# Optimization experiments

Hardware: AMD Instinct MI355X
Metric: run time of the kernel (lower is better)

The kernel has to match this reference:

```python
import jax, jax.numpy as jnp
import numpy as np

B, DIM, H, W = 4, 512, 64, 64
HEADS = 8
MAX_FREQ = 10000.0


def _rope_cos_sin(h, w, head_dim, dtype):
    # 2D RoPE: first quarter of half_dim uses row position, second quarter uses col position
    half = head_dim // 2
    quarter = half // 2
    pos_h = jnp.arange(h, dtype=dtype)
    pos_w = jnp.arange(w, dtype=dtype)
    gh, gw = jnp.meshgrid(pos_h, pos_w, indexing='ij')
    pos = jnp.stack([gh.ravel(), gw.ravel()], axis=-1)  # [N, 2]
    freqs = 1.0 / (MAX_FREQ ** (jnp.arange(quarter, dtype=dtype) / quarter))  # [quarter]
    ang_x = pos[:, 0:1] * freqs  # [N, quarter]
    ang_y = pos[:, 1:2] * freqs  # [N, quarter]
    cos = jnp.concatenate([jnp.cos(ang_x), jnp.cos(ang_y)], axis=-1)  # [N, half]
    sin = jnp.concatenate([jnp.sin(ang_x), jnp.sin(ang_y)], axis=-1)  # [N, half]
    return cos, sin


def _apply_rope(x, cos, sin):
    # x: [B, heads, N, head_dim]; cos/sin: [N, head_dim//2]
    d = x.shape[-1] // 2
    x1, x2 = x[..., :d], x[..., d:]
    return jnp.concatenate([x1 * cos - x2 * sin, x1 * sin + x2 * cos], axis=-1)


def setup_inputs() -> dict:
    key = jax.random.key(0)
    kx, kq, kp = jax.random.split(key, 3)
    x = jax.random.normal(kx, (B, DIM, H, W), dtype=jnp.float32)
    w_qkv = jax.random.normal(kq, (3 * DIM, DIM), dtype=jnp.float32) * (DIM ** -0.5)
    w_proj = jax.random.normal(kp, (DIM, DIM), dtype=jnp.float32) * (DIM ** -0.5)
    return {"x": x, "w_qkv": w_qkv, "w_proj": w_proj}


def reference(x, w_qkv, w_proj):
    Bb, C, Hh, Ww = x.shape
    heads = HEADS
    hd = C // heads
    N = Hh * Ww
    # 1x1 conv (bias-free) == channel-wise linear
    qkv = jnp.einsum('bchw,oc->bohw', x, w_qkv)  # [B, 3C, H, W]
    qkv = qkv.reshape(Bb, 3, heads, hd, Hh, Ww).transpose(1, 0, 2, 4, 5, 3)  # [3, B, heads, H, W, hd]
    q = qkv[0].reshape(Bb, heads, N, hd)
    k = qkv[1].reshape(Bb, heads, N, hd)
    v = qkv[2].reshape(Bb, heads, N, hd)
    cos, sin = _rope_cos_sin(Hh, Ww, hd, x.dtype)
    q = _apply_rope(q, cos, sin)
    k = _apply_rope(k, cos, sin)
    scale = hd ** -0.5
    attn = jax.nn.softmax(jnp.einsum('bhnd,bhmd->bhnm', q, k) * scale, axis=-1)  # [B, heads, N, N]
    out = jnp.einsum('bhnm,bhmd->bhnd', attn, v)  # [B, heads, N, hd]
    out = out.reshape(Bb, heads, Hh, Ww, hd).transpose(0, 1, 4, 2, 3).reshape(Bb, C, Hh, Ww)
    return jnp.einsum('bchw,oc->bohw', out, w_proj)
```

## Files before the change

### kernel.cpp

```cpp
#include <hip/hip_runtime.h>
#include <math.h>

#define B_    4
#define CDIM  512
#define HEADS 8
#define HD    64
#define NN    4096
#define QSZ   ((size_t)B_*HEADS*NN*HD)
#define SCALE_Q 0.18033688011112042f

typedef __attribute__((ext_vector_type(8))) short short8;
typedef __attribute__((ext_vector_type(4))) float f32x4;
typedef __attribute__((ext_vector_type(16))) float f32x16;
union U4S8 { uint4 u; short8 s; };

__device__ inline unsigned pk(float a, float b) {
    unsigned ua = __float_as_uint(a), ub = __float_as_uint(b);
    ua += 0x7FFFu + ((ua >> 16) & 1u);
    ub += 0x7FFFu + ((ub >> 16) & 1u);
    return (ua >> 16) | (ub & 0xFFFF0000u);
}
__device__ inline unsigned short bf16_1(float a) {
    unsigned ua = __float_as_uint(a);
    ua += 0x7FFFu + ((ua >> 16) & 1u);
    return (unsigned short)(ua >> 16);
}
__device__ inline unsigned cvtpk(float a, float b) {
    unsigned r;
    asm("v_cvt_pk_bf16_f32 %0, %1, %2" : "=v"(r) : "v"(a), "v"(b));
    return r;
}

__device__ inline void load_lds16(const unsigned short* g, unsigned short* l) {
    __builtin_amdgcn_global_load_lds(
        (const __attribute__((address_space(1))) unsigned int*)g,
        (__attribute__((address_space(3))) unsigned int*)l, 16, 0, 0);
}

__global__ void conv_w_kernel(const float* __restrict__ wq, const float* __restrict__ wp,
                              unsigned short* __restrict__ wqb, unsigned short* __restrict__ wpb) {
    int id = blockIdx.x * 256 + threadIdx.x;
    const float* src; unsigned short* dst; size_t off; float sc = 1.0f;
    if (id < 98304) { src = wq; dst = wqb; off = (size_t)id * 8; if (off < 262144) sc = SCALE_Q; }
    else            { src = wp; dst = wpb; off = (size_t)(id - 98304) * 8; }
    float4 a = *(const float4*)(src + off);
    float4 b = *(const float4*)(src + off + 4);
    uint4 u;
    u.x = pk(a.x * sc, a.y * sc); u.y = pk(a.z * sc, a.w * sc);
    u.z = pk(b.x * sc, b.y * sc); u.w = pk(b.z * sc, b.w * sc);
    *(uint4*)(dst + off) = u;
}

__global__ void rope_table_kernel(float* __restrict__ ct, float* __restrict__ st) {
    int id = blockIdx.x * 256 + threadIdx.x;
    int j = id >> 12, n = id & 4095;
    int i = j & 15;
    float pos = (j < 16) ? (float)(n >> 6) : (float)(n & 63);
    float freq = exp2f(-(float)i * 0.8304820237218406f);
    float ang = pos * freq;
    ct[id] = cosf(ang);
    st[id] = sinf(ang);
}

__global__ __launch_bounds__(256) void transpose_x_kernel(
        const float* __restrict__ x, unsigned short* __restrict__ xt) {
    __shared__ unsigned short T[64 * 72];
    int t = threadIdx.x;
    int b = blockIdx.z, c0 = blockIdx.y * 64, n0 = blockIdx.x * 64;
    const float* xb = x + ((size_t)b * CDIM + c0) * NN + n0;
    int crow = t >> 2, nseg = t & 3;
#pragma unroll
    for (int g = 0; g < 4; ++g) {
        float4 f = *(const float4*)(xb + (size_t)crow * NN + nseg * 16 + g * 4);
        int nb = nseg * 16 + g * 4;
        T[(nb + 0) * 72 + crow] = bf16_1(f.x);
        T[(nb + 1) * 72 + crow] = bf16_1(f.y);
        T[(nb + 2) * 72 + crow] = bf16_1(f.z);
        T[(nb + 3) * 72 + crow] = bf16_1(f.w);
    }
    __syncthreads();
    unsigned short* xo = xt + ((size_t)b * NN + n0) * CDIM + c0;
    int nrow = t >> 2, cseg = t & 3;
    uint4 u0 = *(uint4*)(T + nrow * 72 + cseg * 16);
    uint4 u1 = *(uint4*)(T + nrow * 72 + cseg * 16 + 8);
    *(uint4*)(xo + (size_t)nrow * CDIM + cseg * 16)     = u0;
    *(uint4*)(xo + (size_t)nrow * CDIM + cseg * 16 + 8) = u1;
}

__global__ __launch_bounds__(256, 2) void qkv_mfma_kernel(
        const unsigned short* __restrict__ xt, const unsigned short* __restrict__ wq,
        unsigned short* __restrict__ qbf, unsigned short* __restrict__ kbf,
        unsigned short* __restrict__ vt,
        const float* __restrict__ ct, const float* __restrict__ st) {
    __shared__ unsigned short smem[8192];
    int t = threadIdx.x;
    int lane = t & 63, w = t >> 6;
    int qlo = lane & 15, quad = lane >> 4;
    int b = blockIdx.z, o0 = blockIdx.y * 128, n0 = blockIdx.x * 128;
    const unsigned short* xb = xt + (size_t)b * NN * CDIM;
    int row = t >> 2, seg = t & 3;
    int wn = (w & 1) * 64, wo = (w >> 1) * 64;

    f32x4 acc[4][4];
#pragma unroll
    for (int i = 0; i < 4; ++i)
#pragma unroll
        for (int j = 0; j < 4; ++j) acc[i][j] = f32x4{0.f, 0.f, 0.f, 0.f};

    for (int k0 = 0; k0 < 512; k0 += 32) {
        __syncthreads();
        load_lds16(xb + (size_t)(n0 + row) * 512 + k0 + seg * 8,        smem + t * 8);
        load_lds16(xb + (size_t)(n0 + 64 + row) * 512 + k0 + seg * 8,   smem + 2048 + t * 8);
        load_lds16(wq + (size_t)(o0 + row) * 512 + k0 + seg * 8,        smem + 4096 + t * 8);
        load_lds16(wq + (size_t)(o0 + 64 + row) * 512 + k0 + seg * 8,   smem + 6144 + t * 8);
        __syncthreads();
        U4S8 af[4], bf[4];
#pragma unroll
        for (int mt = 0; mt < 4; ++mt)
            af[mt].u = *(const uint4*)(smem + (wn + 16 * mt + qlo) * 32 + quad * 8);
#pragma unroll
        for (int nt = 0; nt < 4; ++nt)
            bf[nt].u = *(const uint4*)(smem + 4096 + (wo + 16 * nt + qlo) * 32 + quad * 8);
#pragma unroll
        for (int mt = 0; mt < 4; ++mt)
#pragma unroll
            for (int nt = 0; nt < 4; ++nt)
                acc[mt][nt] = __builtin_amdgcn_mfma_f32_16x16x32_bf16(
                    af[mt].s, bf[nt].s, acc[mt][nt], 0, 0, 0);
    }

    int og = o0 + wo;
    int s = og >> 9;
    int h = (og & 511) >> 6;
    int bh = b * HEADS + h;
    if (s < 2) {
        unsigned short* dst = (s ? kbf : qbf) + (size_t)bh * NN * HD;
#pragma unroll
        for (int mt = 0; mt < 4; ++mt) {
            int nbase = n0 + wn + 16 * mt + 4 * quad;
#pragma unroll
            for (int ntp = 0; ntp < 2; ++ntp) {
                int j = 16 * ntp + qlo;
                float4 c4 = *(const float4*)(ct + (size_t)j * NN + nbase);
                float4 s4 = *(const float4*)(st + (size_t)j * NN + nbase);
                float cc[4] = {c4.x, c4.y, c4.z, c4.w};
                float ss[4] = {s4.x, s4.y, s4.z, s4.w};
#pragma unroll
                for (int r = 0; r < 4; ++r) {
                    float x1 = acc[mt][ntp][r], x2 = acc[mt][ntp + 2][r];
                    size_t base = (size_t)(nbase + r) * HD;
                    dst[base + j]      = bf16_1(x1 * cc[r] - x2 * ss[r]);
                    dst[base + j + 32] = bf16_1(x1 * ss[r] + x2 * cc[r]);
                }
            }
        }
    } else {
        unsigned short* dst = vt + (size_t)bh * HD * NN;
#pragma unroll
        for (int mt = 0; mt < 4; ++mt)
#pragma unroll
            for (int nt = 0; nt < 4; ++nt) {
                int d = 16 * nt + qlo;
                int n = n0 + wn + 16 * mt + 4 * quad;
                uint2 u;
                u.x = pk(acc[mt][nt][0], acc[mt][nt][1]);
                u.y = pk(acc[mt][nt][2], acc[mt][nt][3]);
                *(uint2*)(dst + (size_t)d * NN + n) = u;
            }
    }
}

#define EXP_GRP(Sv, MTQ, KSL, PA)                                        \
    {                                                                    \
        float p0 = __builtin_amdgcn_exp2f(Sv[8 * (KSL) + 0]);            \
        float p1 = __builtin_amdgcn_exp2f(Sv[8 * (KSL) + 1]);            \
        float p2 = __builtin_amdgcn_exp2f(Sv[8 * (KSL) + 2]);            \
        float p3 = __builtin_amdgcn_exp2f(Sv[8 * (KSL) + 3]);            \
        float p4 = __builtin_amdgcn_exp2f(Sv[8 * (KSL) + 4]);            \
        float p5 = __builtin_amdgcn_exp2f(Sv[8 * (KSL) + 5]);            \
        float p6 = __builtin_amdgcn_exp2f(Sv[8 * (KSL) + 6]);            \
        float p7 = __builtin_amdgcn_exp2f(Sv[8 * (KSL) + 7]);            \
        Lsum[MTQ] += ((p0 + p1) + (p2 + p3)) + ((p4 + p5) + (p6 + p7));  \
        PA.u.x = cvtpk(p0, p1); PA.u.y = cvtpk(p2, p3);                  \
        PA.u.z = cvtpk(p4, p5); PA.u.w = cvtpk(p6, p7);                  \
    }

__global__ __launch_bounds__(256, 2) void attn_kernel(
        const unsigned short* __restrict__ qbf, const unsigned short* __restrict__ kbf,
        const unsigned short* __restrict__ vt, unsigned short* __restrict__ aot) {
    __shared__ unsigned char smem[36864];
    int t = threadIdx.x;
    int lane = t & 63, w = t >> 6;
    int l31 = lane & 31, h = lane >> 5;
    int bb = blockIdx.z, hh = blockIdx.y;
    int bh = bb * HEADS + hh;
    int n0w = blockIdx.x * 256 + w * 64;

    U4S8 qf[2][4];
    const unsigned short* qg = qbf + ((size_t)bh * NN + n0w) * HD;
#pragma unroll
    for (int mtq = 0; mtq < 2; ++mtq)
#pragma unroll
        for (int ks = 0; ks < 4; ++ks)
            qf[mtq][ks].u = *(const uint4*)(qg + (size_t)(32 * mtq + l31) * 64 + 16 * ks + 8 * h);

    f32x16 Zv;
#pragma unroll
    for (int i = 0; i < 16; ++i) Zv[i] = 0.f;

    f32x16 O[2][2];
#pragma unroll
    for (int mtq = 0; mtq < 2; ++mtq)
#pragma unroll
        for (int ntd = 0; ntd < 2; ++ntd) O[mtq][ntd] = Zv;
    float Lsum[2] = {0.f, 0.f};

    const uint4* kg = (const uint4*)kbf + (size_t)bh * NN * 8;
    const uint4* vg = (const uint4*)vt  + (size_t)bh * 64 * 512;

    int rr0 = t >> 3, s8 = t & 7;
    int voff = 32 * (s8 >> 1) + 8 * (s8 & 1);

    const uint4* kp0 = kg + rr0 * 8 + s8;
    const uint4* kp1 = kg + (32 + rr0) * 8 + s8;
    const uint4* vp0 = vg + rr0 * 512 + s8;
    const uint4* vp1 = vg + (32 + rr0) * 512 + s8;

    unsigned char* kd0 = smem + rr0 * 144 + s8 * 16;
    unsigned char* kd1 = smem + (32 + rr0) * 144 + s8 * 16;
    unsigned char* vd0 = smem + 9216 + rr0 * 144 + voff;
    unsigned char* vd1 = smem + 9216 + (32 + rr0) * 144 + voff;

    uint4 kr0 = kp0[0], kr1 = kp1[0], vr0 = vp0[0], vr1 = vp1[0];
    kp0 += 512; kp1 += 512; vp0 += 8; vp1 += 8;
    *(uint4*)(kd0) = kr0;
    *(uint4*)(kd1) = kr1;
    *(uint2*)(vd0)      = make_uint2(vr0.x, vr0.y);
    *(uint2*)(vd0 + 16) = make_uint2(vr0.z, vr0.w);
    *(uint2*)(vd1)      = make_uint2(vr1.x, vr1.y);
    *(uint2*)(vd1 + 16) = make_uint2(vr1.z, vr1.w);
    kr0 = kp0[0]; kr1 = kp1[0]; vr0 = vp0[0]; vr1 = vp1[0];
    kp0 += 512; kp1 += 512; vp0 += 8; vp1 += 8;
    __syncthreads();

    for (int c = 0; c < NN / 64; ++c) {
        int bo = (c & 1) * 18432;
        const unsigned char* kb  = smem + bo;
        const unsigned char* vbb = smem + bo + 9216;
        int bo2 = bo ^ 18432;

        *(uint4*)(kd0 + bo2) = kr0;
        *(uint4*)(kd1 + bo2) = kr1;
        *(uint2*)(vd0 + bo2)      = make_uint2(vr0.x, vr0.y);
        *(uint2*)(vd0 + bo2 + 16) = make_uint2(vr0.z, vr0.w);
        *(uint2*)(vd1 + bo2)      = make_uint2(vr1.x, vr1.y);
        *(uint2*)(vd1 + bo2 + 16) = make_uint2(vr1.z, vr1.w);
        kr0 = kp0[0]; kr1 = kp1[0]; vr0 = vp0[0]; vr1 = vp1[0];
        kp0 += 512; kp1 += 512; vp0 += 8; vp1 += 8;

        __builtin_amdgcn_s_setprio(1);

        U4S8 ka0[4];
#pragma unroll
        for (int ks = 0; ks < 4; ++ks)
            ka0[ks].u = *(const uint4*)(kb + l31 * 144 + 32 * ks + 16 * h);
        f32x16 S0[2];
        S0[0] = __builtin_amdgcn_mfma_f32_32x32x16_bf16(ka0[0].s, qf[0][0].s, Zv, 0, 0, 0);
        S0[1] = __builtin_amdgcn_mfma_f32_32x32x16_bf16(ka0[0].s, qf[1][0].s, Zv, 0, 0, 0);
#pragma unroll
        for (int ks = 1; ks < 4; ++ks) {
            S0[0] = __builtin_amdgcn_mfma_f32_32x32x16_bf16(ka0[ks].s, qf[0][ks].s, S0[0], 0, 0, 0);
            S0[1] = __builtin_amdgcn_mfma_f32_32x32x16_bf16(ka0[ks].s, qf[1][ks].s, S0[1], 0, 0, 0);
        }

        U4S8 ka1[4];
#pragma unroll
        for (int ks = 0; ks < 4; ++ks)
            ka1[ks].u = *(const uint4*)(kb + (32 + l31) * 144 + 32 * ks + 16 * h);
        f32x16 S1[2];
        U4S8 paA[2][2];
        S1[0] = __builtin_amdgcn_mfma_f32_32x32x16_bf16(ka1[0].s, qf[0][0].s, Zv, 0, 0, 0);
        S1[1] = __builtin_amdgcn_mfma_f32_32x32x16_bf16(ka1[0].s, qf[1][0].s, Zv, 0, 0, 0);
        EXP_GRP(S0[0], 0, 0, paA[0][0]);
        S1[0] = __builtin_amdgcn_mfma_f32_32x32x16_bf16(ka1[1].s, qf[0][1].s, S1[0], 0, 0, 0);
        S1[1] = __builtin_amdgcn_mfma_f32_32x32x16_bf16(ka1[1].s, qf[1][1].s, S1[1], 0, 0, 0);
        EXP_GRP(S0[0], 0, 1, paA[1][0]);
        S1[0] = __builtin_amdgcn_mfma_f32_32x32x16_bf16(ka1[2].s, qf[0][2].s, S1[0], 0, 0, 0);
        S1[1] = __builtin_amdgcn_mfma_f32_32x32x16_bf16(ka1[2].s, qf[1][2].s, S1[1], 0, 0, 0);
        EXP_GRP(S0[1], 1, 0, paA[0][1]);
        S1[0] = __builtin_amdgcn_mfma_f32_32x32x16_bf16(ka1[3].s, qf[0][3].s, S1[0], 0, 0, 0);
        S1[1] = __builtin_amdgcn_mfma_f32_32x32x16_bf16(ka1[3].s, qf[1][3].s, S1[1], 0, 0, 0);
        EXP_GRP(S0[1], 1, 1, paA[1][1]);

        U4S8 paB[2][2];
        {
            U4S8 vb; vb.u = *(const uint4*)(vbb + l31 * 144 + 16 * h);
            O[0][0] = __builtin_amdgcn_mfma_f32_32x32x16_bf16(paA[0][0].s, vb.s, O[0][0], 0, 0, 0);
            O[1][0] = __builtin_amdgcn_mfma_f32_32x32x16_bf16(paA[0][1].s, vb.s, O[1][0], 0, 0, 0);
        }
        EXP_GRP(S1[0], 0, 0, paB[0][0]);
        {
            U4S8 vb; vb.u = *(const uint4*)(vbb + (32 + l31) * 144 + 16 * h);
            O[0][1] = __builtin_amdgcn_mfma_f32_32x32x16_bf16(paA[0][0].s, vb.s, O[0][1], 0, 0, 0);
            O[1][1] = __builtin_amdgcn_mfma_f32_32x32x16_bf16(paA[0][1].s, vb.s, O[1][1], 0, 0, 0);
        }
        EXP_GRP(S1[0], 0, 1, paB[1][0]);
        {
            U4S8 vb; vb.u = *(const uint4*)(vbb + l31 * 144 + 32 + 16 * h);
            O[0][0] = __builtin_amdgcn_mfma_f32_32x32x16_bf16(paA[1][0].s, vb.s, O[0][0], 0, 0, 0);
            O[1][0] = __builtin_amdgcn_mfma_f32_32x32x16_bf16(paA[1][1].s, vb.s, O[1][0], 0, 0, 0);
        }
        EXP_GRP(S1[1], 1, 0, paB[0][1]);
        {
            U4S8 vb; vb.u = *(const uint4*)(vbb + (32 + l31) * 144 + 32 + 16 * h);
            O[0][1] = __builtin_amdgcn_mfma_f32_32x32x16_bf16(paA[1][0].s, vb.s, O[0][1], 0, 0, 0);
            O[1][1] = __builtin_amdgcn_mfma_f32_32x32x16_bf16(paA[1][1].s, vb.s, O[1][1], 0, 0, 0);
        }
        EXP_GRP(S1[1], 1, 1, paB[1][1]);

        {
            U4S8 vb; vb.u = *(const uint4*)(vbb + l31 * 144 + 64 + 16 * h);
            O[0][0] = __builtin_amdgcn_mfma_f32_32x32x16_bf16(paB[0][0].s, vb.s, O[0][0], 0, 0, 0);
            O[1][0] = __builtin_amdgcn_mfma_f32_32x32x16_bf16(paB[0][1].s, vb.s, O[1][0], 0, 0, 0);
        }
        {
            U4S8 vb; vb.u = *(const uint4*)(vbb + (32 + l31) * 144 + 64 + 16 * h);
            O[0][1] = __builtin_amdgcn_mfma_f32_32x32x16_bf16(paB[0][0].s, vb.s, O[0][1], 0, 0, 0);
            O[1][1] = __builtin_amdgcn_mfma_f32_32x32x16_bf16(paB[0][1].s, vb.s, O[1][1], 0, 0, 0);
        }
        {
            U4S8 vb; vb.u = *(const uint4*)(vbb + l31 * 144 + 96 + 16 * h);
            O[0][0] = __builtin_amdgcn_mfma_f32_32x32x16_bf16(paB[1][0].s, vb.s, O[0][0], 0, 0, 0);
            O[1][0] = __builtin_amdgcn_mfma_f32_32x32x16_bf16(paB[1][1].s, vb.s, O[1][0], 0, 0, 0);
        }
        {
            U4S8 vb; vb.u = *(const uint4*)(vbb + (32 + l31) * 144 + 96 + 16 * h);
            O[0][1] = __builtin_amdgcn_mfma_f32_32x32x16_bf16(paB[1][0].s, vb.s, O[0][1], 0, 0, 0);
            O[1][1] = __builtin_amdgcn_mfma_f32_32x32x16_bf16(paB[1][1].s, vb.s, O[1][1], 0, 0, 0);
        }
        __builtin_amdgcn_s_setprio(0);
        __syncthreads();
    }

    float Linv[2];
#pragma unroll
    for (int mtq = 0; mtq < 2; ++mtq) {
        float l = Lsum[mtq] + __shfl_xor(Lsum[mtq], 32, 64);
        Linv[mtq] = 1.0f / l;
    }
    unsigned short* Tw = (unsigned short*)(smem + w * 4608);
    unsigned short* aob = aot + ((size_t)bb * NN) * CDIM + hh * 64;
#pragma unroll
    for (int mtq = 0; mtq < 2; ++mtq) {
        float iv[16];
#pragma unroll
        for (int r = 0; r < 16; ++r) {
            int src = (r & 3) + 8 * ((r >> 2) & 1) + 16 * (r >> 3) + 4 * h;
            iv[r] = __shfl(Linv[mtq], src, 64);
        }
#pragma unroll
        for (int rg = 0; rg < 2; ++rg) {
#pragma unroll
            for (int ntd = 0; ntd < 2; ++ntd)
#pragma unroll
                for (int rr = 0; rr < 8; ++rr) {
                    int r = 8 * rg + rr;
                    int q16 = (rr & 3) + 8 * (rr >> 2) + 4 * h;
                    Tw[q16 * 72 + 32 * ntd + l31] = bf16_1(O[mtq][ntd][r] * iv[r]);
                }
            int row = lane >> 2, cseg = lane & 3;
            uint4 u0 = *(uint4*)(Tw + row * 72 + cseg * 16);
            uint4 u1 = *(uint4*)(Tw + row * 72 + cseg * 16 + 8);
            unsigned short* arow = aob
                + (size_t)(n0w + 32 * mtq + 16 * rg + row) * CDIM + cseg * 16;
            *(uint4*)(arow)     = u0;
            *(uint4*)(arow + 8) = u1;
        }
    }
}

__global__ __launch_bounds__(256, 2) void proj_mfma_kernel(
        const unsigned short* __restrict__ aot, const unsigned short* __restrict__ wp,
        float* __restrict__ out) {
    __shared__ unsigned short smem[8192];
    int t = threadIdx.x;
    int lane = t & 63, w = t >> 6;
    int qlo = lane & 15, quad = lane >> 4;
    int b = blockIdx.z, o0 = blockIdx.y * 128, n0 = blockIdx.x * 128;
    const unsigned short* ab = aot + (size_t)b * NN * CDIM;
    int row = t >> 2, seg = t & 3;
    int wn = (w & 1) * 64, wo = (w >> 1) * 64;

    f32x4 acc[4][4];
#pragma unroll
    for (int i = 0; i < 4; ++i)
#pragma unroll
        for (int j = 0; j < 4; ++j) acc[i][j] = f32x4{0.f, 0.f, 0.f, 0.f};

    for (int k0 = 0; k0 < 512; k0 += 32) {
        __syncthreads();
        load_lds16(ab + (size_t)(n0 + row) * 512 + k0 + seg * 8,        smem + t * 8);
        load_lds16(ab + (size_t)(n0 + 64 + row) * 512 + k0 + seg * 8,   smem + 2048 + t * 8);
        load_lds16(wp + (size_t)(o0 + row) * 512 + k0 + seg * 8,        smem + 4096 + t * 8);
        load_lds16(wp + (size_t)(o0 + 64 + row) * 512 + k0 + seg * 8,   smem + 6144 + t * 8);
        __syncthreads();
        U4S8 af[4], bf[4];
#pragma unroll
        for (int mt = 0; mt < 4; ++mt)
            af[mt].u = *(const uint4*)(smem + (wn + 16 * mt + qlo) * 32 + quad * 8);
#pragma unroll
        for (int nt = 0; nt < 4; ++nt)
            bf[nt].u = *(const uint4*)(smem + 4096 + (wo + 16 * nt + qlo) * 32 + quad * 8);
#pragma unroll
        for (int mt = 0; mt < 4; ++mt)
#pragma unroll
            for (int nt = 0; nt < 4; ++nt)
                acc[mt][nt] = __builtin_amdgcn_mfma_f32_16x16x32_bf16(
                    af[mt].s, bf[nt].s, acc[mt][nt], 0, 0, 0);
    }

    float* ob = out + (size_t)b * CDIM * NN;
#pragma unroll
    for (int mt = 0; mt < 4; ++mt)
#pragma unroll
        for (int nt = 0; nt < 4; ++nt) {
            int o = o0 + wo + 16 * nt + qlo;
            int n = n0 + wn + 16 * mt + 4 * quad;
            *(float4*)(ob + (size_t)o * NN + n) = *(float4*)&acc[mt][nt];
        }
}

extern "C" void kernel_launch(void* const* d_in, const int* in_sizes, int n_in,
                              void* d_out, int out_size, void* d_ws, size_t ws_size,
                              hipStream_t stream) {
    const float* x      = (const float*)d_in[0];
    const float* w_qkv  = (const float*)d_in[1];
    const float* w_proj = (const float*)d_in[2];
    float* out = (float*)d_out;
    unsigned short* ws = (unsigned short*)d_ws;

    unsigned short* xt  = ws;
    unsigned short* qbf = xt  + QSZ;
    unsigned short* kbf = qbf + QSZ;
    unsigned short* vt  = kbf + QSZ;
    unsigned short* aot = vt  + QSZ;
    unsigned short* wqb = aot + QSZ;
    unsigned short* wpb = wqb + 786432;
    float* ct = (float*)(wpb + 262144);
    float* st = ct + 32 * 4096;

    conv_w_kernel<<<512, 256, 0, stream>>>(w_qkv, w_proj, wqb, wpb);
    rope_table_kernel<<<512, 256, 0, stream>>>(ct, st);
    transpose_x_kernel<<<dim3(64, 8, B_), 256, 0, stream>>>(x, xt);
    qkv_mfma_kernel<<<dim3(32, 12, B_), 256, 0, stream>>>(xt, wqb, qbf, kbf, vt, ct, st);
    attn_kernel<<<dim3(NN / 256, HEADS, B_), 256, 0, stream>>>(qbf, kbf, vt, aot);
    proj_mfma_kernel<<<dim3(32, 4, B_), 256, 0, stream>>>(aot, wpb, out);
}
```

Baseline: 279.2 us.

## Software-pipeline QK^T across half-tiles with triple-buffered K/V shared memory

Restructures the attention main loop so the QK^T MFMAs for the next 32-key half-tile are issued together with the exp/softmax and PV MFMAs of the previous half. A steady-state two-stage pipeline results, with a prologue and an epilogue. Shared memory grows from two to three K/V buffers (55 KB) so the next tile can be written while the current and following halves are being read. This adds register pressure from the extra live S tiles and more LDS use, which may lower occupancy given the 2-blocks-per-CU launch bound.

Result: no change. 282.0 us (+1.0%).

```diff
diff --git a/kernel.cpp b/kernel.cpp
--- a/kernel.cpp
+++ b/kernel.cpp
@@ -185,10 +185,46 @@
         PA.u.z = cvtpk(p4, p5); PA.u.w = cvtpk(p6, p7);                  \
     }
 
+#define MFMA32(A, B, C) __builtin_amdgcn_mfma_f32_32x32x16_bf16((A), (B), (C), 0, 0, 0)
+
+#define HALF_STEP(SCONS, SPROD, KBASE, KHALF, VBASE, VHALF)                              \
+    {                                                                                    \
+        U4S8 ka0, ka1, ka2, ka3;                                                         \
+        ka0.u = *(const uint4*)((KBASE) + ((KHALF) * 32 + l31) * 144 + 16 * h);          \
+        ka1.u = *(const uint4*)((KBASE) + ((KHALF) * 32 + l31) * 144 + 32 + 16 * h);     \
+        ka2.u = *(const uint4*)((KBASE) + ((KHALF) * 32 + l31) * 144 + 64 + 16 * h);     \
+        ka3.u = *(const uint4*)((KBASE) + ((KHALF) * 32 + l31) * 144 + 96 + 16 * h);     \
+        U4S8 pa[2][2];                                                                   \
+        SPROD[0] = MFMA32(ka0.s, qf[0][0].s, Zv);                                        \
+        SPROD[1] = MFMA32(ka0.s, qf[1][0].s, Zv);                                        \
+        EXP_GRP(SCONS[0], 0, 0, pa[0][0]);                                               \
+        SPROD[0] = MFMA32(ka1.s, qf[0][1].s, SPROD[0]);                                  \
+        SPROD[1] = MFMA32(ka1.s, qf[1][1].s, SPROD[1]);                                  \
+        EXP_GRP(SCONS[0], 0, 1, pa[1][0]);                                               \
+        SPROD[0] = MFMA32(ka2.s, qf[0][2].s, SPROD[0]);                                  \
+        SPROD[1] = MFMA32(ka2.s, qf[1][2].s, SPROD[1]);                                  \
+        EXP_GRP(SCONS[1], 1, 0, pa[0][1]);                                               \
+        SPROD[0] = MFMA32(ka3.s, qf[0][3].s, SPROD[0]);                                  \
+        SPROD[1] = MFMA32(ka3.s, qf[1][3].s, SPROD[1]);                                  \
+        EXP_GRP(SCONS[1], 1, 1, pa[1][1]);                                               \
+        { U4S8 vb; vb.u = *(const uint4*)((VBASE) + l31 * 144 + (VHALF) * 64 + 16 * h);  \
+          O[0][0] = MFMA32(pa[0][0].s, vb.s, O[0][0]);                                   \
+          O[1][0] = MFMA32(pa[0][1].s, vb.s, O[1][0]); }                                 \
+        { U4S8 vb; vb.u = *(const uint4*)((VBASE) + (32 + l31) * 144 + (VHALF) * 64 + 16 * h); \
+          O[0][1] = MFMA32(pa[0][0].s, vb.s, O[0][1]);                                   \
+          O[1][1] = MFMA32(pa[0][1].s, vb.s, O[1][1]); }                                 \
+        { U4S8 vb; vb.u = *(const uint4*)((VBASE) + l31 * 144 + (VHALF) * 64 + 32 + 16 * h); \
+          O[0][0] = MFMA32(pa[1][0].s, vb.s, O[0][0]);                                   \
+          O[1][0] = MFMA32(pa[1][1].s, vb.s, O[1][0]); }                                 \
+        { U4S8 vb; vb.u = *(const uint4*)((VBASE) + (32 + l31) * 144 + (VHALF) * 64 + 32 + 16 * h); \
+          O[0][1] = MFMA32(pa[1][0].s, vb.s, O[0][1]);                                   \
+          O[1][1] = MFMA32(pa[1][1].s, vb.s, O[1][1]); }                                 \
+    }
+
 __global__ __launch_bounds__(256, 2) void attn_kernel(
         const unsigned short* __restrict__ qbf, const unsigned short* __restrict__ kbf,
         const unsigned short* __restrict__ vt, unsigned short* __restrict__ aot) {
-    __shared__ unsigned char smem[36864];
+    __shared__ unsigned char smem[55296];
     int t = threadIdx.x;
     int lane = t & 63, w = t >> 6;
     int l31 = lane & 31, h = lane >> 5;
@@ -231,115 +267,80 @@
     unsigned char* vd0 = smem + 9216 + rr0 * 144 + voff;
     unsigned char* vd1 = smem + 9216 + (32 + rr0) * 144 + voff;
 
-    uint4 kr0 = kp0[0], kr1 = kp1[0], vr0 = vp0[0], vr1 = vp1[0];
-    kp0 += 512; kp1 += 512; vp0 += 8; vp1 += 8;
-    *(uint4*)(kd0) = kr0;
-    *(uint4*)(kd1) = kr1;
-    *(uint2*)(vd0)      = make_uint2(vr0.x, vr0.y);
-    *(uint2*)(vd0 + 16) = make_uint2(vr0.z, vr0.w);
-    *(uint2*)(vd1)      = make_uint2(vr1.x, vr1.y);
-    *(uint2*)(vd1 + 16) = make_uint2(vr1.z, vr1.w);
+    uint4 kr0, kr1, vr0, vr1;
+#pragma unroll
+    for (int pt = 0; pt < 2; ++pt) {
+        kr0 = kp0[0]; kr1 = kp1[0]; vr0 = vp0[0]; vr1 = vp1[0];
+        kp0 += 512; kp1 += 512; vp0 += 8; vp1 += 8;
+        int bo = pt * 18432;
+        *(uint4*)(kd0 + bo) = kr0;
+        *(uint4*)(kd1 + bo) = kr1;
+        *(uint2*)(vd0 + bo)      = make_uint2(vr0.x, vr0.y);
+        *(uint2*)(vd0 + bo + 16) = make_uint2(vr0.z, vr0.w);
+        *(uint2*)(vd1 + bo)      = make_uint2(vr1.x, vr1.y);
+        *(uint2*)(vd1 + bo + 16) = make_uint2(vr1.z, vr1.w);
+    }
     kr0 = kp0[0]; kr1 = kp1[0]; vr0 = vp0[0]; vr1 = vp1[0];
     kp0 += 512; kp1 += 512; vp0 += 8; vp1 += 8;
     __syncthreads();
 
-    for (int c = 0; c < NN / 64; ++c) {
-        int bo = (c & 1) * 18432;
-        const unsigned char* kb  = smem + bo;
-        const unsigned char* vbb = smem + bo + 9216;
-        int bo2 = bo ^ 18432;
-
-        *(uint4*)(kd0 + bo2) = kr0;
-        *(uint4*)(kd1 + bo2) = kr1;
-        *(uint2*)(vd0 + bo2)      = make_uint2(vr0.x, vr0.y);
-        *(uint2*)(vd0 + bo2 + 16) = make_uint2(vr0.z, vr0.w);
-        *(uint2*)(vd1 + bo2)      = make_uint2(vr1.x, vr1.y);
-        *(uint2*)(vd1 + bo2 + 16) = make_uint2(vr1.z, vr1.w);
+    f32x16 SA[2], SB[2];
+    {
+        U4S8 ka0, ka1, ka2, ka3;
+        ka0.u = *(const uint4*)(smem + l31 * 144 + 16 * h);
+        ka1.u = *(const uint4*)(smem + l31 * 144 + 32 + 16 * h);
+        ka2.u = *(const uint4*)(smem + l31 * 144 + 64 + 16 * h);
+        ka3.u = *(const uint4*)(smem + l31 * 144 + 96 + 16 * h);
+        SB[0] = MFMA32(ka0.s, qf[0][0].s, Zv);
+        SB[1] = MFMA32(ka0.s, qf[1][0].s, Zv);
+        SB[0] = MFMA32(ka1.s, qf[0][1].s, SB[0]);
+        SB[1] = MFMA32(ka1.s, qf[1][1].s, SB[1]);
+        SB[0] = MFMA32(ka2.s, qf[0][2].s, SB[0]);
+        SB[1] = MFMA32(ka2.s, qf[1][2].s, SB[1]);
+        SB[0] = MFMA32(ka3.s, qf[0][3].s, SB[0]);
+        SB[1] = MFMA32(ka3.s, qf[1][3].s, SB[1]);
+    }
+
+    int b0 = 0, b1 = 18432, b2 = 36864;
+    for (int c = 0; c < 63; ++c) {
+        *(uint4*)(kd0 + b2) = kr0;
+        *(uint4*)(kd1 + b2) = kr1;
+        *(uint2*)(vd0 + b2)      = make_uint2(vr0.x, vr0.y);
+        *(uint2*)(vd0 + b2 + 16) = make_uint2(vr0.z, vr0.w);
+        *(uint2*)(vd1 + b2)      = make_uint2(vr1.x, vr1.y);
+        *(uint2*)(vd1 + b2 + 16) = make_uint2(vr1.z, vr1.w);
         kr0 = kp0[0]; kr1 = kp1[0]; vr0 = vp0[0]; vr1 = vp1[0];
         kp0 += 512; kp1 += 512; vp0 += 8; vp1 += 8;
 
         __builtin_amdgcn_s_setprio(1);
-
-        U4S8 ka0[4];
-#pragma unroll
-        for (int ks = 0; ks < 4; ++ks)
-            ka0[ks].u = *(const uint4*)(kb + l31 * 144 + 32 * ks + 16 * h);
-        f32x16 S0[2];
-        S0[0] = __builtin_amdgcn_mfma_f32_32x32x16_bf16(ka0[0].s, qf[0][0].s, Zv, 0, 0, 0);
-        S0[1] = __builtin_amdgcn_mfma_f32_32x32x16_bf16(ka0[0].s, qf[1][0].s, Zv, 0, 0, 0);
-#pragma unroll
-        for (int ks = 1; ks < 4; ++ks) {
-            S0[0] = __builtin_amdgcn_mfma_f32_32x32x16_bf16(ka0[ks].s, qf[0][ks].s, S0[0], 0, 0, 0);
-            S0[1] = __builtin_amdgcn_mfma_f32_32x32x16_bf16(ka0[ks].s, qf[1][ks].s, S0[1], 0, 0, 0);
-        }
-
-        U4S8 ka1[4];
-#pragma unroll
-        for (int ks = 0; ks < 4; ++ks)
-            ka1[ks].u = *(const uint4*)(kb + (32 + l31) * 144 + 32 * ks + 16 * h);
-        f32x16 S1[2];
-        U4S8 paA[2][2];
-        S1[0] = __builtin_amdgcn_mfma_f32_32x32x16_bf16(ka1[0].s, qf[0][0].s, Zv, 0, 0, 0);
-        S1[1] = __builtin_amdgcn_mfma_f32_32x32x16_bf16(ka1[0].s, qf[1][0].s, Zv, 0, 0, 0);
-        EXP_GRP(S0[0], 0, 0, paA[0][0]);
-        S1[0] = __builtin_amdgcn_mfma_f32_32x32x16_bf16(ka1[1].s, qf[0][1].s, S1[0], 0, 0, 0);
-        S1[1] = __builtin_amdgcn_mfma_f32_32x32x16_bf16(ka1[1].s, qf[1][1].s, S1[1], 0, 0, 0);
-        EXP_GRP(S0[0], 0, 1, paA[1][0]);
-        S1[0] = __builtin_amdgcn_mfma_f32_32x32x16_bf16(ka1[2].s, qf[0][2].s, S1[0], 0, 0, 0);
-        S1[1] = __builtin_amdgcn_mfma_f32_32x32x16_bf16(ka1[2].s, qf[1][2].s, S1[1], 0, 0, 0);
-        EXP_GRP(S0[1], 1, 0, paA[0][1]);
-        S1[0] = __builtin_amdgcn_mfma_f32_32x32x16_bf16(ka1[3].s, qf[0][3].s, S1[0], 0, 0, 0);
-        S1[1] = __builtin_amdgcn_mfma_f32_32x32x16_bf16(ka1[3].s, qf[1][3].s, S1[1], 0, 0, 0);
-        EXP_GRP(S0[1], 1, 1, paA[1][1]);
-
-        U4S8 paB[2][2];
-        {
-            U4S8 vb; vb.u = *(const uint4*)(vbb + l31 * 144 + 16 * h);
-            O[0][0] = __builtin_amdgcn_mfma_f32_32x32x16_bf16(paA[0][0].s, vb.s, O[0][0], 0, 0, 0);
-            O[1][0] = __builtin_amdgcn_mfma_f32_32x32x16_bf16(paA[0][1].s, vb.s, O[1][0], 0, 0, 0);
-        }
-        EXP_GRP(S1[0], 0, 0, paB[0][0]);
-        {
-            U4S8 vb; vb.u = *(const uint4*)(vbb + (32 + l31) * 144 + 16 * h);
-            O[0][1] = __builtin_amdgcn_mfma_f32_32x32x16_bf16(paA[0][0].s, vb.s, O[0][1], 0, 0, 0);
-            O[1][1] = __builtin_amdgcn_mfma_f32_32x32x16_bf16(paA[0][1].s, vb.s, O[1][1], 0, 0, 0);
-        }
-        EXP_GRP(S1[0], 0, 1, paB[1][0]);
-        {
-            U4S8 vb; vb.u = *(const uint4*)(vbb + l31 * 144 + 32 + 16 * h);
-            O[0][0] = __builtin_amdgcn_mfma_f32_32x32x16_bf16(paA[1][0].s, vb.s, O[0][0], 0, 0, 0);
-            O[1][0] = __builtin_amdgcn_mfma_f32_32x32x16_bf16(paA[1][1].s, vb.s, O[1][0], 0, 0, 0);
-        }
-        EXP_GRP(S1[1], 1, 0, paB[0][1]);
-        {
-            U4S8 vb; vb.u = *(const uint4*)(vbb + (32 + l31) * 144 + 32 + 16 * h);
-            O[0][1] = __builtin_amdgcn_mfma_f32_32x32x16_bf16(paA[1][0].s, vb.s, O[0][1], 0, 0, 0);
-            O[1][1] = __builtin_amdgcn_mfma_f32_32x32x16_bf16(paA[1][1].s, vb.s, O[1][1], 0, 0, 0);
-        }
-        EXP_GRP(S1[1], 1, 1, paB[1][1]);
-
-        {
-            U4S8 vb; vb.u = *(const uint4*)(vbb + l31 * 144 + 64 + 16 * h);
-            O[0][0] = __builtin_amdgcn_mfma_f32_32x32x16_bf16(paB[0][0].s, vb.s, O[0][0], 0, 0, 0);
-            O[1][0] = __builtin_amdgcn_mfma_f32_32x32x16_bf16(paB[0][1].s, vb.s, O[1][0], 0, 0, 0);
-        }
-        {
-            U4S8 vb; vb.u = *(const uint4*)(vbb + (32 + l31) * 144 + 64 + 16 * h);
-            O[0][1] = __builtin_amdgcn_mfma_f32_32x32x16_bf16(paB[0][0].s, vb.s, O[0][1], 0, 0, 0);
-            O[1][1] = __builtin_amdgcn_mfma_f32_32x32x16_bf16(paB[0][1].s, vb.s, O[1][1], 0, 0, 0);
-        }
-        {
-            U4S8 vb; vb.u = *(const uint4*)(vbb + l31 * 144 + 96 + 16 * h);
-            O[0][0] = __builtin_amdgcn_mfma_f32_32x32x16_bf16(paB[1][0].s, vb.s, O[0][0], 0, 0, 0);
-            O[1][0] = __builtin_amdgcn_mfma_f32_32x32x16_bf16(paB[1][1].s, vb.s, O[1][0], 0, 0, 0);
-        }
-        {
-            U4S8 vb; vb.u = *(const uint4*)(vbb + (32 + l31) * 144 + 96 + 16 * h);
-            O[0][1] = __builtin_amdgcn_mfma_f32_32x32x16_bf16(paB[1][0].s, vb.s, O[0][1], 0, 0, 0);
-            O[1][1] = __builtin_amdgcn_mfma_f32_32x32x16_bf16(paB[1][1].s, vb.s, O[1][1], 0, 0, 0);
-        }
+        HALF_STEP(SB, SA, smem + b0, 1, smem + b0 + 9216, 0)
+        HALF_STEP(SA, SB, smem + b1, 0, smem + b0 + 9216, 1)
         __builtin_amdgcn_s_setprio(0);
+
+        int tmp = b0; b0 = b1; b1 = b2; b2 = tmp;
         __syncthreads();
+    }
+
+    HALF_STEP(SB, SA, smem + b0, 1, smem + b0 + 9216, 0)
+    {
+        U4S8 pa[2][2];
+        EXP_GRP(SA[0], 0, 0, pa[0][0]);
+        EXP_GRP(SA[0], 0, 1, pa[1][0]);
+        EXP_GRP(SA[1], 1, 0, pa[0][1]);
+        EXP_GRP(SA[1], 1, 1, pa[1][1]);
+        const unsigned char* vbb = smem + b0 + 9216;
+        { U4S8 vb; vb.u = *(const uint4*)(vbb + l31 * 144 + 64 + 16 * h);
+          O[0][0] = MFMA32(pa[0][0].s, vb.s, O[0][0]);
+          O[1][0] = MFMA32(pa[0][1].s, vb.s, O[1][0]); }
+        { U4S8 vb; vb.u = *(const uint4*)(vbb + (32 + l31) * 144 + 64 + 16 * h);
+          O[0][1] = MFMA32(pa[0][0].s, vb.s, O[0][1]);
+          O[1][1] = MFMA32(pa[0][1].s, vb.s, O[1][1]); }
+        { U4S8 vb; vb.u = *(const uint4*)(vbb + l31 * 144 + 96 + 16 * h);
+          O[0][0] = MFMA32(pa[1][0].s, vb.s, O[0][0]);
+          O[1][0] = MFMA32(pa[1][1].s, vb.s, O[1][0]); }
+        { U4S8 vb; vb.u = *(const uint4*)(vbb + (32 + l31) * 144 + 96 + 16 * h);
+          O[0][1] = MFMA32(pa[1][0].s, vb.s, O[0][1]);
+          O[1][1] = MFMA32(pa[1][1].s, vb.s, O[1][1]); }
     }
 
     float Linv[2];
@@ -348,6 +349,7 @@
         float l = Lsum[mtq] + __shfl_xor(Lsum[mtq], 32, 64);
         Linv[mtq] = 1.0f / l;
     }
+    __syncthreads();
     unsigned short* Tw = (unsigned short*)(smem + w * 4608);
     unsigned short* aob = aot + ((size_t)bb * NN) * CDIM + hh * 64;
 #pragma unroll
```

## Double-buffer swizzled GEMM LDS stages and shrink attention query tile per wave

Applied to the files above, without the earlier changes.

The QKV and projection GEMMs now stage 64-wide K slices into two LDS buffers. An XOR swizzle avoids bank conflicts, and the next slice is prefetched while the current one is computed, which removes one barrier per step. The attention kernel drops from 64 to 32 query rows per wave and 128 per block, and launches twice as many blocks with a higher occupancy hint. This cuts register pressure so more waves can hide latency, at the cost of loading each K/V tile into LDS twice as often per query. The GEMM kernels also use four times as much LDS, which may limit how many blocks can be resident.

After: 296.7 us. 1.06x slower.

```diff
diff --git a/kernel.cpp b/kernel.cpp
--- a/kernel.cpp
+++ b/kernel.cpp
@@ -87,18 +87,56 @@
     *(uint4*)(xo + (size_t)nrow * CDIM + cseg * 16 + 8) = u1;
 }
 
-__global__ __launch_bounds__(256, 2) void qkv_mfma_kernel(
+#define GEMM_STAGE(SRC_A, SRC_B, ST, K0)                                               \
+    {                                                                                  \
+        unsigned short* sdst = smem + (ST) * 16384;                                    \
+        _Pragma("unroll")                                                              \
+        for (int i = 0; i < 4; ++i) {                                                  \
+            int R  = 32 * i + row;                                                     \
+            int sg = (seg ^ (R & 7)) * 8;                                              \
+            load_lds16((SRC_A) + (size_t)(n0 + R) * 512 + (K0) + sg,                   \
+                       sdst + i * 2048 + t * 8);                                       \
+            load_lds16((SRC_B) + (size_t)(o0 + R) * 512 + (K0) + sg,                   \
+                       sdst + 8192 + i * 2048 + t * 8);                                \
+        }                                                                              \
+    }
+
+#define GEMM_KSTEP(SB)                                                                 \
+    _Pragma("unroll")                                                                  \
+    for (int kk = 0; kk < 2; ++kk) {                                                   \
+        U4S8 af[4], bf4[4];                                                            \
+        _Pragma("unroll")                                                              \
+        for (int mt = 0; mt < 4; ++mt) {                                               \
+            int R = wn + 16 * mt + qlo;                                                \
+            af[mt].u = *(const uint4*)((SB) + R * 64 +                                 \
+                        ((kk * 32 + quad * 8) ^ ((R & 7) * 8)));                       \
+        }                                                                              \
+        _Pragma("unroll")                                                              \
+        for (int nt = 0; nt < 4; ++nt) {                                               \
+            int R = wo + 16 * nt + qlo;                                                \
+            bf4[nt].u = *(const uint4*)((SB) + 8192 + R * 64 +                         \
+                        ((kk * 32 + quad * 8) ^ ((R & 7) * 8)));                       \
+        }                                                                              \
+        _Pragma("unroll")                                                              \
+        for (int mt = 0; mt < 4; ++mt)                                                 \
+            _Pragma("unroll")                                                          \
+            for (int nt = 0; nt < 4; ++nt)                                             \
+                acc[mt][nt] = __builtin_amdgcn_mfma_f32_16x16x32_bf16(                 \
+                    af[mt].s, bf4[nt].s, acc[mt][nt], 0, 0, 0);                        \
+    }
+
+__global__ __launch_bounds__(256, 3) void qkv_mfma_kernel(
         const unsigned short* __restrict__ xt, const unsigned short* __restrict__ wq,
         unsigned short* __restrict__ qbf, unsigned short* __restrict__ kbf,
         unsigned short* __restrict__ vt,
         const float* __restrict__ ct, const float* __restrict__ st) {
-    __shared__ unsigned short smem[8192];
+    __shared__ unsigned short smem[32768];
     int t = threadIdx.x;
     int lane = t & 63, w = t >> 6;
     int qlo = lane & 15, quad = lane >> 4;
     int b = blockIdx.z, o0 = blockIdx.y * 128, n0 = blockIdx.x * 128;
     const unsigned short* xb = xt + (size_t)b * NN * CDIM;
-    int row = t >> 2, seg = t & 3;
+    int row = t >> 3, seg = t & 7;
     int wn = (w & 1) * 64, wo = (w >> 1) * 64;
 
     f32x4 acc[4][4];
@@ -107,26 +145,12 @@
 #pragma unroll
         for (int j = 0; j < 4; ++j) acc[i][j] = f32x4{0.f, 0.f, 0.f, 0.f};
 
-    for (int k0 = 0; k0 < 512; k0 += 32) {
+    GEMM_STAGE(xb, wq, 0, 0)
+    for (int it = 0; it < 8; ++it) {
         __syncthreads();
-        load_lds16(xb + (size_t)(n0 + row) * 512 + k0 + seg * 8,        smem + t * 8);
-        load_lds16(xb + (size_t)(n0 + 64 + row) * 512 + k0 + seg * 8,   smem + 2048 + t * 8);
-        load_lds16(wq + (size_t)(o0 + row) * 512 + k0 + seg * 8,        smem + 4096 + t * 8);
-        load_lds16(wq + (size_t)(o0 + 64 + row) * 512 + k0 + seg * 8,   smem + 6144 + t * 8);
-        __syncthreads();
-        U4S8 af[4], bf[4];
-#pragma unroll
-        for (int mt = 0; mt < 4; ++mt)
-            af[mt].u = *(const uint4*)(smem + (wn + 16 * mt + qlo) * 32 + quad * 8);
-#pragma unroll
-        for (int nt = 0; nt < 4; ++nt)
-            bf[nt].u = *(const uint4*)(smem + 4096 + (wo + 16 * nt + qlo) * 32 + quad * 8);
-#pragma unroll
-        for (int mt = 0; mt < 4; ++mt)
-#pragma unroll
-            for (int nt = 0; nt < 4; ++nt)
-                acc[mt][nt] = __builtin_amdgcn_mfma_f32_16x16x32_bf16(
-                    af[mt].s, bf[nt].s, acc[mt][nt], 0, 0, 0);
+        if (it < 7) GEMM_STAGE(xb, wq, (it + 1) & 1, (it + 1) * 64)
+        const unsigned short* s = smem + (it & 1) * 16384;
+        GEMM_KSTEP(s)
     }
 
     int og = o0 + wo;
@@ -170,7 +194,7 @@
     }
 }
 
-#define EXP_GRP(Sv, MTQ, KSL, PA)                                        \
+#define EXP_GRP1(Sv, KSL, PA)                                            \
     {                                                                    \
         float p0 = __builtin_amdgcn_exp2f(Sv[8 * (KSL) + 0]);            \
         float p1 = __builtin_amdgcn_exp2f(Sv[8 * (KSL) + 1]);            \
@@ -180,12 +204,14 @@
         float p5 = __builtin_amdgcn_exp2f(Sv[8 * (KSL) + 5]);            \
         float p6 = __builtin_amdgcn_exp2f(Sv[8 * (KSL) + 6]);            \
         float p7 = __builtin_amdgcn_exp2f(Sv[8 * (KSL) + 7]);            \
-        Lsum[MTQ] += ((p0 + p1) + (p2 + p3)) + ((p4 + p5) + (p6 + p7));  \
+        Lsum += ((p0 + p1) + (p2 + p3)) + ((p4 + p5) + (p6 + p7));       \
         PA.u.x = cvtpk(p0, p1); PA.u.y = cvtpk(p2, p3);                  \
         PA.u.z = cvtpk(p4, p5); PA.u.w = cvtpk(p6, p7);                  \
     }
 
-__global__ __launch_bounds__(256, 2) void attn_kernel(
+#define MFMA32(A, B, C) __builtin_amdgcn_mfma_f32_32x32x16_bf16((A), (B), (C), 0, 0, 0)
+
+__global__ __launch_bounds__(256, 4) void attn_kernel(
         const unsigned short* __restrict__ qbf, const unsigned short* __restrict__ kbf,
         const unsigned short* __restrict__ vt, unsigned short* __restrict__ aot) {
     __shared__ unsigned char smem[36864];
@@ -194,26 +220,21 @@
     int l31 = lane & 31, h = lane >> 5;
     int bb = blockIdx.z, hh = blockIdx.y;
     int bh = bb * HEADS + hh;
-    int n0w = blockIdx.x * 256 + w * 64;
-
-    U4S8 qf[2][4];
+    int n0w = blockIdx.x * 128 + w * 32;
+
+    U4S8 qf[4];
     const unsigned short* qg = qbf + ((size_t)bh * NN + n0w) * HD;
 #pragma unroll
-    for (int mtq = 0; mtq < 2; ++mtq)
-#pragma unroll
-        for (int ks = 0; ks < 4; ++ks)
-            qf[mtq][ks].u = *(const uint4*)(qg + (size_t)(32 * mtq + l31) * 64 + 16 * ks + 8 * h);
+    for (int ks = 0; ks < 4; ++ks)
+        qf[ks].u = *(const uint4*)(qg + (size_t)l31 * 64 + 16 * ks + 8 * h);
 
     f32x16 Zv;
 #pragma unroll
     for (int i = 0; i < 16; ++i) Zv[i] = 0.f;
 
-    f32x16 O[2][2];
-#pragma unroll
-    for (int mtq = 0; mtq < 2; ++mtq)
-#pragma unroll
-        for (int ntd = 0; ntd < 2; ++ntd) O[mtq][ntd] = Zv;
-    float Lsum[2] = {0.f, 0.f};
+    f32x16 O[2];
+    O[0] = Zv; O[1] = Zv;
+    float Lsum = 0.f;
 
     const uint4* kg = (const uint4*)kbf + (size_t)bh * NN * 8;
     const uint4* vg = (const uint4*)vt  + (size_t)bh * 64 * 512;
@@ -264,131 +285,108 @@
 #pragma unroll
         for (int ks = 0; ks < 4; ++ks)
             ka0[ks].u = *(const uint4*)(kb + l31 * 144 + 32 * ks + 16 * h);
-        f32x16 S0[2];
-        S0[0] = __builtin_amdgcn_mfma_f32_32x32x16_bf16(ka0[0].s, qf[0][0].s, Zv, 0, 0, 0);
-        S0[1] = __builtin_amdgcn_mfma_f32_32x32x16_bf16(ka0[0].s, qf[1][0].s, Zv, 0, 0, 0);
-#pragma unroll
-        for (int ks = 1; ks < 4; ++ks) {
-            S0[0] = __builtin_amdgcn_mfma_f32_32x32x16_bf16(ka0[ks].s, qf[0][ks].s, S0[0], 0, 0, 0);
-            S0[1] = __builtin_amdgcn_mfma_f32_32x32x16_bf16(ka0[ks].s, qf[1][ks].s, S0[1], 0, 0, 0);
-        }
+        f32x16 S0;
+        S0 = MFMA32(ka0[0].s, qf[0].s, Zv);
+        S0 = MFMA32(ka0[1].s, qf[1].s, S0);
+        S0 = MFMA32(ka0[2].s, qf[2].s, S0);
+        S0 = MFMA32(ka0[3].s, qf[3].s, S0);
 
         U4S8 ka1[4];
 #pragma unroll
         for (int ks = 0; ks < 4; ++ks)
             ka1[ks].u = *(const uint4*)(kb + (32 + l31) * 144 + 32 * ks + 16 * h);
-        f32x16 S1[2];
-        U4S8 paA[2][2];
-        S1[0] = __builtin_amdgcn_mfma_f32_32x32x16_bf16(ka1[0].s, qf[0][0].s, Zv, 0, 0, 0);
-        S1[1] = __builtin_amdgcn_mfma_f32_32x32x16_bf16(ka1[0].s, qf[1][0].s, Zv, 0, 0, 0);
-        EXP_GRP(S0[0], 0, 0, paA[0][0]);
-        S1[0] = __builtin_amdgcn_mfma_f32_32x32x16_bf16(ka1[1].s, qf[0][1].s, S1[0], 0, 0, 0);
-        S1[1] = __builtin_amdgcn_mfma_f32_32x32x16_bf16(ka1[1].s, qf[1][1].s, S1[1], 0, 0, 0);
-        EXP_GRP(S0[0], 0, 1, paA[1][0]);
-        S1[0] = __builtin_amdgcn_mfma_f32_32x32x16_bf16(ka1[2].s, qf[0][2].s, S1[0], 0, 0, 0);
-        S1[1] = __builtin_amdgcn_mfma_f32_32x32x16_bf16(ka1[2].s, qf[1][2].s, S1[1], 0, 0, 0);
-        EXP_GRP(S0[1], 1, 0, paA[0][1]);
-        S1[0] = __builtin_amdgcn_mfma_f32_32x32x16_bf16(ka1[3].s, qf[0][3].s, S1[0], 0, 0, 0);
-        S1[1] = __builtin_amdgcn_mfma_f32_32x32x16_bf16(ka1[3].s, qf[1][3].s, S1[1], 0, 0, 0);
-        EXP_GRP(S0[1], 1, 1, paA[1][1]);
-
-        U4S8 paB[2][2];
+        f32x16 S1;
+        U4S8 paA[2];
+        S1 = MFMA32(ka1[0].s, qf[0].s, Zv);
+        S1 = MFMA32(ka1[1].s, qf[1].s, S1);
+        EXP_GRP1(S0, 0, paA[0]);
+        S1 = MFMA32(ka1[2].s, qf[2].s, S1);
+        EXP_GRP1(S0, 1, paA[1]);
+        S1 = MFMA32(ka1[3].s, qf[3].s, S1);
+
+        U4S8 paB[2];
         {
             U4S8 vb; vb.u = *(const uint4*)(vbb + l31 * 144 + 16 * h);
-            O[0][0] = __builtin_amdgcn_mfma_f32_32x32x16_bf16(paA[0][0].s, vb.s, O[0][0], 0, 0, 0);
-            O[1][0] = __builtin_amdgcn_mfma_f32_32x32x16_bf16(paA[0][1].s, vb.s, O[1][0], 0, 0, 0);
-        }
-        EXP_GRP(S1[0], 0, 0, paB[0][0]);
+            O[0] = MFMA32(paA[0].s, vb.s, O[0]);
+        }
+        EXP_GRP1(S1, 0, paB[0]);
         {
             U4S8 vb; vb.u = *(const uint4*)(vbb + (32 + l31) * 144 + 16 * h);
-            O[0][1] = __builtin_amdgcn_mfma_f32_32x32x16_bf16(paA[0][0].s, vb.s, O[0][1], 0, 0, 0);
-            O[1][1] = __builtin_amdgcn_mfma_f32_32x32x16_bf16(paA[0][1].s, vb.s, O[1][1], 0, 0, 0);
-        }
-        EXP_GRP(S1[0], 0, 1, paB[1][0]);
+            O[1] = MFMA32(paA[0].s, vb.s, O[1]);
+        }
+        EXP_GRP1(S1, 1, paB[1]);
         {
             U4S8 vb; vb.u = *(const uint4*)(vbb + l31 * 144 + 32 + 16 * h);
-            O[0][0] = __builtin_amdgcn_mfma_f32_32x32x16_bf16(paA[1][0].s, vb.s, O[0][0], 0, 0, 0);
-            O[1][0] = __builtin_amdgcn_mfma_f32_32x32x16_bf16(paA[1][1].s, vb.s, O[1][0], 0, 0, 0);
-        }
-        EXP_GRP(S1[1], 1, 0, paB[0][1]);
+            O[0] = MFMA32(paA[1].s, vb.s, O[0]);
+        }
         {
             U4S8 vb; vb.u = *(const uint4*)(vbb + (32 + l31) * 144 + 32 + 16 * h);
-            O[0][1] = __builtin_amdgcn_mfma_f32_32x32x16_bf16(paA[1][0].s, vb.s, O[0][1], 0, 0, 0);
-            O[1][1] = __builtin_amdgcn_mfma_f32_32x32x16_bf16(paA[1][1].s, vb.s, O[1][1], 0, 0, 0);
-        }
-        EXP_GRP(S1[1], 1, 1, paB[1][1]);
+            O[1] = MFMA32(paA[1].s, vb.s, O[1]);
+        }
 
         {
             U4S8 vb; vb.u = *(const uint4*)(vbb + l31 * 144 + 64 + 16 * h);
-            O[0][0] = __builtin_amdgcn_mfma_f32_32x32x16_bf16(paB[0][0].s, vb.s, O[0][0], 0, 0, 0);
-            O[1][0] = __builtin_amdgcn_mfma_f32_32x32x16_bf16(paB[0][1].s, vb.s, O[1][0], 0, 0, 0);
+            O[0] = MFMA32(paB[0].s, vb.s, O[0]);
         }
         {
             U4S8 vb; vb.u = *(const uint4*)(vbb + (32 + l31) * 144 + 64 + 16 * h);
-            O[0][1] = __builtin_amdgcn_mfma_f32_32x32x16_bf16(paB[0][0].s, vb.s, O[0][1], 0, 0, 0);
-            O[1][1] = __builtin_amdgcn_mfma_f32_32x32x16_bf16(paB[0][1].s, vb.s, O[1][1], 0, 0, 0);
+            O[1] = MFMA32(paB[0].s, vb.s, O[1]);
         }
         {
             U4S8 vb; vb.u = *(const uint4*)(vbb + l31 * 144 + 96 + 16 * h);
-            O[0][0] = __builtin_amdgcn_mfma_f32_32x32x16_bf16(paB[1][0].s, vb.s, O[0][0], 0, 0, 0);
-            O[1][0] = __builtin_amdgcn_mfma_f32_32x32x16_bf16(paB[1][1].s, vb.s, O[1][0], 0, 0, 0);
+            O[0] = MFMA32(paB[1].s, vb.s, O[0]);
         }
         {
             U4S8 vb; vb.u = *(const uint4*)(vbb + (32 + l31) * 144 + 96 + 16 * h);
-            O[0][1] = __builtin_amdgcn_mfma_f32_32x32x16_bf16(paB[1][0].s, vb.s, O[0][1], 0, 0, 0);
-            O[1][1] = __builtin_amdgcn_mfma_f32_32x32x16_bf16(paB[1][1].s, vb.s, O[1][1], 0, 0, 0);
+            O[1] = MFMA32(paB[1].s, vb.s, O[1]);
         }
         __builtin_amdgcn_s_setprio(0);
         __syncthreads();
     }
 
-    float Linv[2];
-#pragma unroll
-    for (int mtq = 0; mtq < 2; ++mtq) {
-        float l = Lsum[mtq] + __shfl_xor(Lsum[mtq], 32, 64);
-        Linv[mtq] = 1.0f / l;
+    float Linv;
+    {
+        float l = Lsum + __shfl_xor(Lsum, 32, 64);
+        Linv = 1.0f / l;
     }
     unsigned short* Tw = (unsigned short*)(smem + w * 4608);
     unsigned short* aob = aot + ((size_t)bb * NN) * CDIM + hh * 64;
-#pragma unroll
-    for (int mtq = 0; mtq < 2; ++mtq) {
-        float iv[16];
-#pragma unroll
-        for (int r = 0; r < 16; ++r) {
-            int src = (r & 3) + 8 * ((r >> 2) & 1) + 16 * (r >> 3) + 4 * h;
-            iv[r] = __shfl(Linv[mtq], src, 64);
-        }
-#pragma unroll
-        for (int rg = 0; rg < 2; ++rg) {
-#pragma unroll
-            for (int ntd = 0; ntd < 2; ++ntd)
-#pragma unroll
-                for (int rr = 0; rr < 8; ++rr) {
-                    int r = 8 * rg + rr;
-                    int q16 = (rr & 3) + 8 * (rr >> 2) + 4 * h;
-                    Tw[q16 * 72 + 32 * ntd + l31] = bf16_1(O[mtq][ntd][r] * iv[r]);
-                }
-            int row = lane >> 2, cseg = lane & 3;
-            uint4 u0 = *(uint4*)(Tw + row * 72 + cseg * 16);
-            uint4 u1 = *(uint4*)(Tw + row * 72 + cseg * 16 + 8);
-            unsigned short* arow = aob
-                + (size_t)(n0w + 32 * mtq + 16 * rg + row) * CDIM + cseg * 16;
-            *(uint4*)(arow)     = u0;
-            *(uint4*)(arow + 8) = u1;
-        }
-    }
-}
-
-__global__ __launch_bounds__(256, 2) void proj_mfma_kernel(
+    float iv[16];
+#pragma unroll
+    for (int r = 0; r < 16; ++r) {
+        int src = (r & 3) + 8 * ((r >> 2) & 1) + 16 * (r >> 3) + 4 * h;
+        iv[r] = __shfl(Linv, src, 64);
+    }
+#pragma unroll
+    for (int rg = 0; rg < 2; ++rg) {
+#pragma unroll
+        for (int ntd = 0; ntd < 2; ++ntd)
+#pragma unroll
+            for (int rr = 0; rr < 8; ++rr) {
+                int r = 8 * rg + rr;
+                int q16 = (rr & 3) + 8 * (rr >> 2) + 4 * h;
+                Tw[q16 * 72 + 32 * ntd + l31] = bf16_1(O[ntd][r] * iv[r]);
+            }
+        int row = lane >> 2, cseg = lane & 3;
+        uint4 u0 = *(uint4*)(Tw + row * 72 + cseg * 16);
+        uint4 u1 = *(uint4*)(Tw + row * 72 + cseg * 16 + 8);
+        unsigned short* arow = aob
+            + (size_t)(n0w + 16 * rg + row) * CDIM + cseg * 16;
+        *(uint4*)(arow)     = u0;
+        *(uint4*)(arow + 8) = u1;
+    }
+}
+
+__global__ __launch_bounds__(256, 3) void proj_mfma_kernel(
         const unsigned short* __restrict__ aot, const unsigned short* __restrict__ wp,
         float* __restrict__ out) {
-    __shared__ unsigned short smem[8192];
+    __shared__ unsigned short smem[32768];
     int t = threadIdx.x;
     int lane = t & 63, w = t >> 6;
     int qlo = lane & 15, quad = lane >> 4;
     int b = blockIdx.z, o0 = blockIdx.y * 128, n0 = blockIdx.x * 128;
     const unsigned short* ab = aot + (size_t)b * NN * CDIM;
-    int row = t >> 2, seg = t & 3;
+    int row = t >> 3, seg = t & 7;
     int wn = (w & 1) * 64, wo = (w >> 1) * 64;
 
     f32x4 acc[4][4];
@@ -397,26 +395,12 @@
 #pragma unroll
         for (int j = 0; j < 4; ++j) acc[i][j] = f32x4{0.f, 0.f, 0.f, 0.f};
 
-    for (int k0 = 0; k0 < 512; k0 += 32) {
+    GEMM_STAGE(ab, wp, 0, 0)
+    for (int it = 0; it < 8; ++it) {
         __syncthreads();
-        load_lds16(ab + (size_t)(n0 + row) * 512 + k0 + seg * 8,        smem + t * 8);
-        load_lds16(ab + (size_t)(n0 + 64 + row) * 512 + k0 + seg * 8,   smem + 2048 + t * 8);
-        load_lds16(wp + (size_t)(o0 + row) * 512 + k0 + seg * 8,        smem + 4096 + t * 8);
-        load_lds16(wp + (size_t)(o0 + 64 + row) * 512 + k0 + seg * 8,   smem + 6144 + t * 8);
-        __syncthreads();
-        U4S8 af[4], bf[4];
-#pragma unroll
-        for (int mt = 0; mt < 4; ++mt)
-            af[mt].u = *(const uint4*)(smem + (wn + 16 * mt + qlo) * 32 + quad * 8);
-#pragma unroll
-        for (int nt = 0; nt < 4; ++nt)
-            bf[nt].u = *(const uint4*)(smem + 4096 + (wo + 16 * nt + qlo) * 32 + quad * 8);
-#pragma unroll
-        for (int mt = 0; mt < 4; ++mt)
-#pragma unroll
-            for (int nt = 0; nt < 4; ++nt)
-                acc[mt][nt] = __builtin_amdgcn_mfma_f32_16x16x32_bf16(
-                    af[mt].s, bf[nt].s, acc[mt][nt], 0, 0, 0);
+        if (it < 7) GEMM_STAGE(ab, wp, (it + 1) & 1, (it + 1) * 64)
+        const unsigned short* s = smem + (it & 1) * 16384;
+        GEMM_KSTEP(s)
     }
 
     float* ob = out + (size_t)b * CDIM * NN;
@@ -453,6 +437,6 @@
     rope_table_kernel<<<512, 256, 0, stream>>>(ct, st);
     transpose_x_kernel<<<dim3(64, 8, B_), 256, 0, stream>>>(x, xt);
     qkv_mfma_kernel<<<dim3(32, 12, B_), 256, 0, stream>>>(xt, wqb, qbf, kbf, vt, ct, st);
-    attn_kernel<<<dim3(NN / 256, HEADS, B_), 256, 0, stream>>>(qbf, kbf, vt, aot);
+    attn_kernel<<<dim3(NN / 128, HEADS, B_), 256, 0, stream>>>(qbf, kbf, vt, aot);
     proj_mfma_kernel<<<dim3(32, 4, B_), 256, 0, stream>>>(aot, wpb, out);
 }
```
